# Performance work log

Measured on AMD Instinct MI355X. Metric: run time of the kernel, lower is better.

## Reference

```python
import jax, jax.numpy as jnp
import numpy as np

N, NFEAT, NHID, NCLASS, NHEADS = 4096, 512, 64, 40, 8
ALPHA = 0.2
NEG = -9e15


def setup_inputs() -> dict:
    key = jax.random.key(0)
    ks = jax.random.split(key, 6)
    x = jax.random.normal(ks[0], (N, NFEAT), dtype=jnp.float32)
    adj = jax.random.randint(ks[1], (2, N, N), 0, 2, dtype=jnp.int32)
    # Xavier-ish scaled params
    W1 = jax.random.normal(ks[2], (NHEADS, NFEAT, NHID), dtype=jnp.float32) * (1.0 / np.sqrt(NFEAT))
    a1 = jax.random.normal(ks[3], (NHEADS, 2, NHID), dtype=jnp.float32) * (1.0 / np.sqrt(2 * NHID))
    Wo = jax.random.normal(ks[4], (NHEADS * NHID, NCLASS), dtype=jnp.float32) * (1.0 / np.sqrt(NHEADS * NHID))
    ao = jax.random.normal(ks[5], (2, NCLASS), dtype=jnp.float32) * (1.0 / np.sqrt(2 * NCLASS))
    return {"x": x, "adj": adj, "W1": W1, "a1": a1, "Wo": Wo, "ao": ao}


def _gat_layer(h, adj_mask, W, a_src, a_dst, concat):
    # h: [N,F]; W: [...,F,F']; a_src/a_dst: [...,F']
    if W.ndim == 3:  # multi-head: [H,F,F']
        Wh = jnp.einsum('nf,hfd->hnd', h, W)              # [H,N,F']
        f1 = jnp.einsum('hnd,hd->hn', Wh, a_src)           # [H,N]
        f2 = jnp.einsum('hnd,hd->hn', Wh, a_dst)
        e = jax.nn.leaky_relu(f1[:, :, None] + f2[:, None, :], ALPHA)  # [H,N,N]
        e = jnp.where(adj_mask[None], e, NEG)
        att = jax.nn.softmax(e, axis=-1)
        out = jnp.einsum('hnm,hmd->hnd', att, Wh)          # [H,N,F']
    else:
        Wh = h @ W                                         # [N,F']
        f1 = Wh @ a_src
        f2 = Wh @ a_dst
        e = jax.nn.leaky_relu(f1[:, None] + f2[None, :], ALPHA)
        e = jnp.where(adj_mask, e, NEG)
        att = jax.nn.softmax(e, axis=-1)
        out = att @ Wh
    return jax.nn.elu(out) if concat else out


def reference(x, adj, W1, a1, Wo, ao):
    adj1 = adj[1] > 0
    adj0 = adj[0] > 0
    # layer 1: NHEADS heads, concat=True
    h = _gat_layer(x, adj1, W1, a1[:, 0], a1[:, 1], concat=True)   # [H,N,NHID]
    h = jnp.transpose(h, (1, 0, 2)).reshape(x.shape[0], -1)        # [N, H*NHID]
    # output layer: concat=False, then outer ELU + log_softmax
    out = _gat_layer(h, adj0, Wo, ao[0], ao[1], concat=False)      # [N, NCLASS]
    out = jax.nn.elu(out)
    return jax.nn.log_softmax(out, axis=1)
```

## Files before the change

kernel.cpp:

```cpp
#include <hip/hip_runtime.h>
#include <hip/hip_bf16.h>

#define N      4096
#define NFEAT  512
#define NHID   64
#define NHEADS 8
#define NCLASS 40
#define ALPHA  0.2f

typedef unsigned short u16;
typedef unsigned int   u32;
typedef __attribute__((ext_vector_type(8))) short bf16x8;
typedef __attribute__((ext_vector_type(4))) float f32x4;

__device__ __forceinline__ float lrelu(float v) {
    return v > 0.f ? v : ALPHA * v;
}
__device__ __forceinline__ u16 f2b(float f) {
    u32 u = __float_as_uint(f);
    return (u16)((u + 0x7FFFu + ((u >> 16) & 1u)) >> 16);
}

__global__ __launch_bounds__(256) void k1_gemm1(const float* __restrict__ x,
                                                const float* __restrict__ W1,
                                                float* __restrict__ Wh1) {
    __shared__ float As[16][64];
    __shared__ float Bs[16][64];
    const int t  = threadIdx.x;
    const int n0 = blockIdx.x * 64;
    const int h  = blockIdx.y;
    const int ti = t >> 4, tj = t & 15;
    const int an = t >> 2;
    const int af = (t & 3) * 4;
    const int bf = t >> 4;
    const int bd = (t & 15) * 4;
    float acc[4][4] = {};
    for (int f0 = 0; f0 < NFEAT; f0 += 16) {
        __syncthreads();
        float4 av = *(const float4*)&x[(size_t)(n0 + an) * NFEAT + f0 + af];
        As[af + 0][an] = av.x;
        As[af + 1][an] = av.y;
        As[af + 2][an] = av.z;
        As[af + 3][an] = av.w;
        *(float4*)&Bs[bf][bd] =
            *(const float4*)&W1[(size_t)h * NFEAT * NHID + (size_t)(f0 + bf) * NHID + bd];
        __syncthreads();
        #pragma unroll
        for (int kf = 0; kf < 16; ++kf) {
            float4 a4 = *(const float4*)&As[kf][ti * 4];
            float4 b4 = *(const float4*)&Bs[kf][tj * 4];
            acc[0][0] += a4.x * b4.x; acc[0][1] += a4.x * b4.y; acc[0][2] += a4.x * b4.z; acc[0][3] += a4.x * b4.w;
            acc[1][0] += a4.y * b4.x; acc[1][1] += a4.y * b4.y; acc[1][2] += a4.y * b4.z; acc[1][3] += a4.y * b4.w;
            acc[2][0] += a4.z * b4.x; acc[2][1] += a4.z * b4.y; acc[2][2] += a4.z * b4.z; acc[2][3] += a4.z * b4.w;
            acc[3][0] += a4.w * b4.x; acc[3][1] += a4.w * b4.y; acc[3][2] += a4.w * b4.z; acc[3][3] += a4.w * b4.w;
        }
    }
    #pragma unroll
    for (int i = 0; i < 4; ++i) {
        *(float4*)&Wh1[(size_t)(n0 + ti * 4 + i) * (NHEADS * NHID) + h * NHID + tj * 4] =
            make_float4(acc[i][0], acc[i][1], acc[i][2], acc[i][3]);
    }
}

__global__ __launch_bounds__(256) void k2_f12(const float* __restrict__ Wh1,
                                              const float* __restrict__ a1,
                                              float* __restrict__ f1,
                                              float* __restrict__ f2) {
    const int t = threadIdx.x;
    const int lane = t & 63;
    const int u = blockIdx.x * 4 + (t >> 6);
    const int h = u >> 12;
    const int n = u & (N - 1);
    float v  = Wh1[(size_t)n * 512 + h * 64 + lane];
    float s1 = v * a1[h * 128 + lane];
    float s2 = v * a1[h * 128 + 64 + lane];
    #pragma unroll
    for (int off = 32; off >= 1; off >>= 1) {
        s1 += __shfl_xor(s1, off);
        s2 += __shfl_xor(s2, off);
    }
    if (lane == 0) { f1[h * N + n] = s1; f2[h * N + n] = s2; }
}

__global__ __launch_bounds__(256) void k2t_transpose(const float* __restrict__ Wh1,
                                                     u16* __restrict__ Wh1T) {
    __shared__ float ts[64 * 68];
    const int t  = threadIdx.x;
    const int m0 = blockIdx.x * 64;
    const int h  = blockIdx.y;
    #pragma unroll
    for (int i = 0; i < 4; ++i) {
        int flat = t + 256 * i;
        int row = flat >> 4;
        int c4  = (flat & 15) * 4;
        *(float4*)&ts[row * 68 + c4] =
            *(const float4*)&Wh1[(size_t)(m0 + row) * 512 + h * 64 + c4];
    }
    __syncthreads();
    const int d  = t >> 2;
    const int ms = (t & 3) * 16;
    u32 p[8];
    #pragma unroll
    for (int j = 0; j < 8; ++j) {
        float v0 = ts[(ms + 2 * j) * 68 + d];
        float v1 = ts[(ms + 2 * j + 1) * 68 + d];
        p[j] = (u32)f2b(v0) | ((u32)f2b(v1) << 16);
    }
    u32* dst = (u32*)&Wh1T[((size_t)(h * 64 + d)) * 4096 + m0 + ms];
    *(uint4*)dst       = make_uint4(p[0], p[1], p[2], p[3]);
    *(uint4*)(dst + 4) = make_uint4(p[4], p[5], p[6], p[7]);
}

__global__ __launch_bounds__(256, 4) void k3_attn1(const int* __restrict__ adj1,
                                                   const u16* __restrict__ Wh1T,
                                                   const float* __restrict__ f1,
                                                   const float* __restrict__ f2,
                                                   float* __restrict__ pacc1,
                                                   float* __restrict__ pz1) {
    __shared__ u16  wbf[64 * 136];
    __shared__ u16  whT[80 * 136];
    __shared__ float f1s[64];
    const int t     = threadIdx.x;
    const int n0    = blockIdx.x * 64;
    const int h     = blockIdx.y;
    const int chunk = blockIdx.z;
    const int lane  = t & 63;
    const int wrow  = (t >> 6) * 16;
    const int c4    = (t & 31) * 4;
    const int rg    = t >> 5;
    if (t < 64) f1s[t] = f1[h * N + n0 + t];
    #pragma unroll
    for (int i = 0; i < 9; ++i) {
        int flat = t + 256 * i;
        if (flat < 16 * 136) {
            int row = 64 + flat / 136;
            whT[row * 136 + (flat % 136)] = (row == 64) ? (u16)0x3F80 : (u16)0;
        }
    }
    f32x4 acc[5];
    #pragma unroll
    for (int df = 0; df < 5; ++df)
        #pragma unroll
        for (int r = 0; r < 4; ++r) acc[df][r] = 0.f;
    __syncthreads();

    const int mbeg = chunk * 2048;
    for (int m0 = mbeg; m0 < mbeg + 2048; m0 += 128) {
        float4 f2v = *(const float4*)&f2[h * N + m0 + c4];
        #pragma unroll
        for (int i = 0; i < 8; ++i) {
            int rr = rg + 8 * i;
            int4 a4 = *(const int4*)&adj1[(size_t)(n0 + rr) * N + m0 + c4];
            float f1v = f1s[rr];
            float w0 = a4.x ? __expf(lrelu(f1v + f2v.x)) : 0.f;
            float w1 = a4.y ? __expf(lrelu(f1v + f2v.y)) : 0.f;
            float w2 = a4.z ? __expf(lrelu(f1v + f2v.z)) : 0.f;
            float w3 = a4.w ? __expf(lrelu(f1v + f2v.w)) : 0.f;
            uint2 pk;
            pk.x = (u32)f2b(w0) | ((u32)f2b(w1) << 16);
            pk.y = (u32)f2b(w2) | ((u32)f2b(w3) << 16);
            *(uint2*)&wbf[rr * 136 + c4] = pk;
        }
        #pragma unroll
        for (int i = 0; i < 4; ++i) {
            int flat = t + 256 * i;
            int row = flat >> 4;
            int c8  = (flat & 15) * 8;
            *(uint4*)&whT[row * 136 + c8] =
                *(const uint4*)&Wh1T[((size_t)(h * 64 + row)) * 4096 + m0 + c8];
        }
        __syncthreads();
        const int ar   = wrow + (lane & 15);
        const int koff = (lane >> 4) * 8;
        #pragma unroll
        for (int ks = 0; ks < 4; ++ks) {
            int k0 = ks * 32 + koff;
            bf16x8 a = *(const bf16x8*)&wbf[ar * 136 + k0];
            #pragma unroll
            for (int df = 0; df < 5; ++df) {
                bf16x8 b = *(const bf16x8*)&whT[(df * 16 + (lane & 15)) * 136 + k0];
                acc[df] = __builtin_amdgcn_mfma_f32_16x16x32_bf16(a, b, acc[df], 0, 0, 0);
            }
        }
        __syncthreads();
    }
    const size_t rowbase = (size_t)(chunk * 8 + h) * 4096 + n0;
    #pragma unroll
    for (int r = 0; r < 4; ++r) {
        int nl = wrow + (lane >> 4) * 4 + r;
        float z = __shfl(acc[4][r], lane & 48);
        if ((lane & 15) == 0) pz1[rowbase + nl] = z;
        #pragma unroll
        for (int df = 0; df < 4; ++df)
            pacc1[(rowbase + nl) * 64 + df * 16 + (lane & 15)] = acc[df][r];
    }
}

__global__ __launch_bounds__(256) void k3b_norm(const float* __restrict__ pacc1,
                                                const float* __restrict__ pz1,
                                                float* __restrict__ h1) {
    const int g = blockIdx.x * 256 + threadIdx.x;
    const int d = g & 63;
    const int h = (g >> 6) & 7;
    const int n = g >> 9;
    const size_t i0 = (size_t)h * 4096 + n;
    float s = pacc1[i0 * 64 + d] + pacc1[(i0 + 8 * 4096) * 64 + d];
    float z = pz1[i0] + pz1[i0 + 8 * 4096];
    float v = s / fmaxf(z, 1e-30f);
    h1[(size_t)n * 512 + h * 64 + d] = v > 0.f ? v : __expf(v) - 1.f;
}

__global__ __launch_bounds__(256) void k4_gemm2(const float* __restrict__ h1,
                                                const float* __restrict__ Wo,
                                                float* __restrict__ Wh2) {
    const int t = threadIdx.x;
    const int c = t & 63;
    const int n = blockIdx.x * 4 + (t >> 6);
    if (c < NCLASS) {
        const float* hrow = &h1[(size_t)n * 512];
        float acc = 0.f;
        #pragma unroll 8
        for (int f = 0; f < 512; ++f)
            acc += hrow[f] * Wo[f * NCLASS + c];
        Wh2[(size_t)n * NCLASS + c] = acc;
    }
}

__global__ __launch_bounds__(256) void k4b_fo(const float* __restrict__ Wh2,
                                              const float* __restrict__ ao,
                                              float* __restrict__ f1o,
                                              float* __restrict__ f2o,
                                              u16* __restrict__ Wh2T) {
    const int n = blockIdx.x * 256 + threadIdx.x;
    float s1 = 0.f, s2 = 0.f;
    #pragma unroll
    for (int c = 0; c < NCLASS; ++c) {
        float v = Wh2[(size_t)n * NCLASS + c];
        s1 += v * ao[c];
        s2 += v * ao[NCLASS + c];
        Wh2T[(size_t)c * 4096 + n] = f2b(v);
    }
    f1o[n] = s1; f2o[n] = s2;
}

__global__ __launch_bounds__(256, 4) void k5a_attn2(const int* __restrict__ adj0,
                                                    const u16* __restrict__ Wh2T,
                                                    const float* __restrict__ f1o,
                                                    const float* __restrict__ f2o,
                                                    float* __restrict__ pacc,
                                                    float* __restrict__ pz) {
    __shared__ u16  wbf[64 * 136];
    __shared__ u16  whT[64 * 136];
    __shared__ float f1s[64];
    const int t     = threadIdx.x;
    const int n0    = blockIdx.x * 64;
    const int chunk = blockIdx.y;
    const int mbase = chunk * 256;
    const int lane  = t & 63;
    const int wrow  = (t >> 6) * 16;
    const int c4    = (t & 31) * 4;
    const int rg    = t >> 5;
    if (t < 64) f1s[t] = f1o[n0 + t];
    #pragma unroll
    for (int i = 0; i < 13; ++i) {
        int flat = t + 256 * i;
        if (flat < 24 * 136) {
            int row = 40 + flat / 136;
            whT[row * 136 + (flat % 136)] = (row == 48) ? (u16)0x3F80 : (u16)0;
        }
    }
    f32x4 acc[4];
    #pragma unroll
    for (int df = 0; df < 4; ++df)
        #pragma unroll
        for (int r = 0; r < 4; ++r) acc[df][r] = 0.f;
    __syncthreads();

    for (int mt = 0; mt < 2; ++mt) {
        int m0 = mbase + mt * 128;
        float4 f2v = *(const float4*)&f2o[m0 + c4];
        #pragma unroll
        for (int i = 0; i < 8; ++i) {
            int rr = rg + 8 * i;
            int4 a4 = *(const int4*)&adj0[(size_t)(n0 + rr) * N + m0 + c4];
            float f1v = f1s[rr];
            float w0 = a4.x ? __expf(lrelu(f1v + f2v.x)) : 0.f;
            float w1 = a4.y ? __expf(lrelu(f1v + f2v.y)) : 0.f;
            float w2 = a4.z ? __expf(lrelu(f1v + f2v.z)) : 0.f;
            float w3 = a4.w ? __expf(lrelu(f1v + f2v.w)) : 0.f;
            uint2 pk;
            pk.x = (u32)f2b(w0) | ((u32)f2b(w1) << 16);
            pk.y = (u32)f2b(w2) | ((u32)f2b(w3) << 16);
            *(uint2*)&wbf[rr * 136 + c4] = pk;
        }
        #pragma unroll
        for (int i = 0; i < 3; ++i) {
            int flat = t + 256 * i;
            if (flat < 640) {
                int row = flat >> 4;
                int c8  = (flat & 15) * 8;
                *(uint4*)&whT[row * 136 + c8] =
                    *(const uint4*)&Wh2T[(size_t)row * 4096 + m0 + c8];
            }
        }
        __syncthreads();
        const int ar   = wrow + (lane & 15);
        const int koff = (lane >> 4) * 8;
        #pragma unroll
        for (int ks = 0; ks < 4; ++ks) {
            int k0 = ks * 32 + koff;
            bf16x8 a = *(const bf16x8*)&wbf[ar * 136 + k0];
            #pragma unroll
            for (int df = 0; df < 4; ++df) {
                bf16x8 b = *(const bf16x8*)&whT[(df * 16 + (lane & 15)) * 136 + k0];
                acc[df] = __builtin_amdgcn_mfma_f32_16x16x32_bf16(a, b, acc[df], 0, 0, 0);
            }
        }
        __syncthreads();
    }
    #pragma unroll
    for (int r = 0; r < 4; ++r) {
        int n = n0 + wrow + (lane >> 4) * 4 + r;
        float z = __shfl(acc[3][r], lane & 48);
        if ((lane & 15) == 0) pz[(size_t)chunk * N + n] = z;
        #pragma unroll
        for (int df = 0; df < 3; ++df) {
            int c = df * 16 + (lane & 15);
            if (c < NCLASS)
                pacc[((size_t)chunk * N + n) * NCLASS + c] = acc[df][r];
        }
    }
}

__global__ __launch_bounds__(256) void k5b_final(const float* __restrict__ pacc,
                                                 const float* __restrict__ pz,
                                                 float* __restrict__ out) {
    const int t = threadIdx.x;
    const int lane = t & 63;
    const int n = blockIdx.x * 4 + (t >> 6);
    float s = 0.f, Z = 0.f;
    #pragma unroll
    for (int ch = 0; ch < 16; ++ch) {
        Z += pz[(size_t)ch * N + n];
        if (lane < NCLASS) s += pacc[((size_t)ch * N + n) * NCLASS + lane];
    }
    float v;
    if (lane < NCLASS) {
        v = s / fmaxf(Z, 1e-30f);
        v = v > 0.f ? v : __expf(v) - 1.f;
    } else {
        v = -INFINITY;
    }
    float mx = v;
    #pragma unroll
    for (int off = 32; off >= 1; off >>= 1) mx = fmaxf(mx, __shfl_xor(mx, off));
    float ex = (lane < NCLASS) ? __expf(v - mx) : 0.f;
    #pragma unroll
    for (int off = 32; off >= 1; off >>= 1) ex += __shfl_xor(ex, off);
    float lse = mx + __logf(ex);
    if (lane < NCLASS) out[(size_t)n * NCLASS + lane] = v - lse;
}

extern "C" void kernel_launch(void* const* d_in, const int* in_sizes, int n_in,
                              void* d_out, int out_size, void* d_ws, size_t ws_size,
                              hipStream_t stream) {
    const float* x   = (const float*)d_in[0];
    const int*   adj = (const int*)d_in[1];
    const float* W1  = (const float*)d_in[2];
    const float* a1  = (const float*)d_in[3];
    const float* Wo  = (const float*)d_in[4];
    const float* ao  = (const float*)d_in[5];

    float* ws    = (float*)d_ws;
    float* h1    = ws;
    float* f1    = h1 + 2097152;
    float* f2    = f1 + 32768;
    float* Wh2   = f2 + 32768;
    float* f1o   = Wh2 + 163840;
    float* f2o   = f1o + 4096;
    float* pz    = f2o + 4096;
    float* pz1   = pz + 65536;
    u16*   Wh1T  = (u16*)(pz1 + 65536);
    u16*   Wh2T  = Wh1T + 2097152;
    float* R     = (float*)(Wh2T + 163840);
    float* Wh1   = R;
    float* pacc1 = R;
    float* pacc  = R;

    const int* adj0 = adj;
    const int* adj1 = adj + (size_t)N * N;

    hipLaunchKernelGGL(k1_gemm1,      dim3(64, 8),    dim3(256), 0, stream, x, W1, Wh1);
    hipLaunchKernelGGL(k2_f12,        dim3(8192),     dim3(256), 0, stream, Wh1, a1, f1, f2);
    hipLaunchKernelGGL(k2t_transpose, dim3(64, 8),    dim3(256), 0, stream, Wh1, Wh1T);
    hipLaunchKernelGGL(k3_attn1,      dim3(64, 8, 2), dim3(256), 0, stream, adj1, Wh1T, f1, f2, pacc1, pz1);
    hipLaunchKernelGGL(k3b_norm,      dim3(8192),     dim3(256), 0, stream, pacc1, pz1, h1);
    hipLaunchKernelGGL(k4_gemm2,      dim3(1024),     dim3(256), 0, stream, h1, Wo, Wh2);
    hipLaunchKernelGGL(k4b_fo,        dim3(16),       dim3(256), 0, stream, Wh2, ao, f1o, f2o, Wh2T);
    hipLaunchKernelGGL(k5a_attn2,     dim3(64, 16),   dim3(256), 0, stream, adj0, Wh2T, f1o, f2o, pacc, pz);
    hipLaunchKernelGGL(k5b_final,     dim3(1024),     dim3(256), 0, stream, pacc, pz, (float*)d_out);
}
```

Measured before the change: 348.4 us.

## Move first GEMM to bf16 MFMA and compute attention weights in registers

The first-layer projection now runs as a bf16 MFMA GEMM on pre-converted x and W1, writing the transposed bf16 Wh1T directly. This replaces the fp32 FMA GEMM and the separate transpose pass, and f1/f2 are then read from Wh1T. Both attention kernels build their exp weights straight into MFMA A-operand registers instead of staging them through shared memory. They also prefetch the Wh tile into registers before the barrier, use exp2 with LOG2E folded into the logits, and raise the occupancy hint to 5. The cost is that the projection is now computed in bf16 instead of fp32, adding rounding error, and two extra conversion kernels are launched.

```diff
diff --git a/kernel.cpp b/kernel.cpp
--- a/kernel.cpp
+++ b/kernel.cpp
@@ -7,86 +7,44 @@
 #define NHEADS 8
 #define NCLASS 40
 #define ALPHA  0.2f
+#define LOG2E  1.44269504f
 
 typedef unsigned short u16;
 typedef unsigned int   u32;
 typedef __attribute__((ext_vector_type(8))) short bf16x8;
 typedef __attribute__((ext_vector_type(4))) float f32x4;
 
-__device__ __forceinline__ float lrelu(float v) {
-    return v > 0.f ? v : ALPHA * v;
+__device__ __forceinline__ float b2f(u16 u) {
+    return __uint_as_float(((u32)u) << 16);
+}
+__device__ __forceinline__ u32 rnd_hi(float f) {
+    u32 u = __float_as_uint(f);
+    return u + 0x7FFFu + ((u >> 16) & 1u);
+}
+__device__ __forceinline__ u32 pkbf(float lo, float hi) {
+    return __builtin_amdgcn_perm(rnd_hi(hi), rnd_hi(lo), 0x07060302);
 }
 __device__ __forceinline__ u16 f2b(float f) {
-    u32 u = __float_as_uint(f);
-    return (u16)((u + 0x7FFFu + ((u >> 16) & 1u)) >> 16);
-}
-
-__global__ __launch_bounds__(256) void k1_gemm1(const float* __restrict__ x,
-                                                const float* __restrict__ W1,
-                                                float* __restrict__ Wh1) {
-    __shared__ float As[16][64];
-    __shared__ float Bs[16][64];
-    const int t  = threadIdx.x;
-    const int n0 = blockIdx.x * 64;
-    const int h  = blockIdx.y;
-    const int ti = t >> 4, tj = t & 15;
-    const int an = t >> 2;
-    const int af = (t & 3) * 4;
-    const int bf = t >> 4;
-    const int bd = (t & 15) * 4;
-    float acc[4][4] = {};
-    for (int f0 = 0; f0 < NFEAT; f0 += 16) {
-        __syncthreads();
-        float4 av = *(const float4*)&x[(size_t)(n0 + an) * NFEAT + f0 + af];
-        As[af + 0][an] = av.x;
-        As[af + 1][an] = av.y;
-        As[af + 2][an] = av.z;
-        As[af + 3][an] = av.w;
-        *(float4*)&Bs[bf][bd] =
-            *(const float4*)&W1[(size_t)h * NFEAT * NHID + (size_t)(f0 + bf) * NHID + bd];
-        __syncthreads();
-        #pragma unroll
-        for (int kf = 0; kf < 16; ++kf) {
-            float4 a4 = *(const float4*)&As[kf][ti * 4];
-            float4 b4 = *(const float4*)&Bs[kf][tj * 4];
-            acc[0][0] += a4.x * b4.x; acc[0][1] += a4.x * b4.y; acc[0][2] += a4.x * b4.z; acc[0][3] += a4.x * b4.w;
-            acc[1][0] += a4.y * b4.x; acc[1][1] += a4.y * b4.y; acc[1][2] += a4.y * b4.z; acc[1][3] += a4.y * b4.w;
-            acc[2][0] += a4.z * b4.x; acc[2][1] += a4.z * b4.y; acc[2][2] += a4.z * b4.z; acc[2][3] += a4.z * b4.w;
-            acc[3][0] += a4.w * b4.x; acc[3][1] += a4.w * b4.y; acc[3][2] += a4.w * b4.z; acc[3][3] += a4.w * b4.w;
-        }
-    }
-    #pragma unroll
-    for (int i = 0; i < 4; ++i) {
-        *(float4*)&Wh1[(size_t)(n0 + ti * 4 + i) * (NHEADS * NHID) + h * NHID + tj * 4] =
-            make_float4(acc[i][0], acc[i][1], acc[i][2], acc[i][3]);
-    }
-}
-
-__global__ __launch_bounds__(256) void k2_f12(const float* __restrict__ Wh1,
-                                              const float* __restrict__ a1,
-                                              float* __restrict__ f1,
-                                              float* __restrict__ f2) {
-    const int t = threadIdx.x;
-    const int lane = t & 63;
-    const int u = blockIdx.x * 4 + (t >> 6);
-    const int h = u >> 12;
-    const int n = u & (N - 1);
-    float v  = Wh1[(size_t)n * 512 + h * 64 + lane];
-    float s1 = v * a1[h * 128 + lane];
-    float s2 = v * a1[h * 128 + 64 + lane];
-    #pragma unroll
-    for (int off = 32; off >= 1; off >>= 1) {
-        s1 += __shfl_xor(s1, off);
-        s2 += __shfl_xor(s2, off);
-    }
-    if (lane == 0) { f1[h * N + n] = s1; f2[h * N + n] = s2; }
-}
-
-__global__ __launch_bounds__(256) void k2t_transpose(const float* __restrict__ Wh1,
-                                                     u16* __restrict__ Wh1T) {
+    return (u16)(rnd_hi(f) >> 16);
+}
+
+__global__ __launch_bounds__(256) void kcx(const float* __restrict__ x,
+                                           u16* __restrict__ xb) {
+    const int g = blockIdx.x * 256 + threadIdx.x;
+    const size_t base = (size_t)g * 8;
+    float4 v0 = *(const float4*)&x[base];
+    float4 v1 = *(const float4*)&x[base + 4];
+    uint4 o;
+    o.x = pkbf(v0.x, v0.y); o.y = pkbf(v0.z, v0.w);
+    o.z = pkbf(v1.x, v1.y); o.w = pkbf(v1.z, v1.w);
+    *(uint4*)&xb[base] = o;
+}
+
+__global__ __launch_bounds__(256) void kcw(const float* __restrict__ W1,
+                                           u16* __restrict__ W1b) {
     __shared__ float ts[64 * 68];
     const int t  = threadIdx.x;
-    const int m0 = blockIdx.x * 64;
+    const int f0 = blockIdx.x * 64;
     const int h  = blockIdx.y;
     #pragma unroll
     for (int i = 0; i < 4; ++i) {
@@ -94,41 +52,111 @@
         int row = flat >> 4;
         int c4  = (flat & 15) * 4;
         *(float4*)&ts[row * 68 + c4] =
-            *(const float4*)&Wh1[(size_t)(m0 + row) * 512 + h * 64 + c4];
+            *(const float4*)&W1[((size_t)h * 512 + f0 + row) * 64 + c4];
     }
     __syncthreads();
     const int d  = t >> 2;
-    const int ms = (t & 3) * 16;
+    const int fs = (t & 3) * 16;
     u32 p[8];
     #pragma unroll
-    for (int j = 0; j < 8; ++j) {
-        float v0 = ts[(ms + 2 * j) * 68 + d];
-        float v1 = ts[(ms + 2 * j + 1) * 68 + d];
-        p[j] = (u32)f2b(v0) | ((u32)f2b(v1) << 16);
-    }
-    u32* dst = (u32*)&Wh1T[((size_t)(h * 64 + d)) * 4096 + m0 + ms];
+    for (int j = 0; j < 8; ++j)
+        p[j] = pkbf(ts[(fs + 2 * j) * 68 + d], ts[(fs + 2 * j + 1) * 68 + d]);
+    u32* dst = (u32*)&W1b[((size_t)(h * 64 + d)) * 512 + f0 + fs];
     *(uint4*)dst       = make_uint4(p[0], p[1], p[2], p[3]);
     *(uint4*)(dst + 4) = make_uint4(p[4], p[5], p[6], p[7]);
 }
 
-__global__ __launch_bounds__(256, 4) void k3_attn1(const int* __restrict__ adj1,
+__global__ __launch_bounds__(256, 4) void k1m_gemm1(const u16* __restrict__ xb,
+                                                    const u16* __restrict__ W1b,
+                                                    u16* __restrict__ Wh1T) {
+    __shared__ u16 xs[64 * 72];
+    __shared__ u16 wvs[64 * 72];
+    const int t    = threadIdx.x;
+    const int n0   = blockIdx.x * 64;
+    const int h    = blockIdx.y;
+    const int lane = t & 63;
+    const int l15  = lane & 15;
+    const int q    = lane >> 4;
+    const int wrow = (t >> 6) * 16;
+    f32x4 acc[4];
+    #pragma unroll
+    for (int df = 0; df < 4; ++df)
+        #pragma unroll
+        for (int r = 0; r < 4; ++r) acc[df][r] = 0.f;
+    for (int f0 = 0; f0 < 512; f0 += 64) {
+        uint4 sx[2], sw[2];
+        #pragma unroll
+        for (int i = 0; i < 2; ++i) {
+            int flat = t + 256 * i;
+            int row = flat >> 3;
+            int c8  = (flat & 7) * 8;
+            sx[i] = *(const uint4*)&xb[(size_t)(n0 + row) * 512 + f0 + c8];
+            sw[i] = *(const uint4*)&W1b[((size_t)(h * 64 + row)) * 512 + f0 + c8];
+        }
+        __syncthreads();
+        #pragma unroll
+        for (int i = 0; i < 2; ++i) {
+            int flat = t + 256 * i;
+            int row = flat >> 3;
+            int c8  = (flat & 7) * 8;
+            *(uint4*)&xs[row * 72 + c8]  = sx[i];
+            *(uint4*)&wvs[row * 72 + c8] = sw[i];
+        }
+        __syncthreads();
+        #pragma unroll
+        for (int ks = 0; ks < 2; ++ks) {
+            int k0 = ks * 32 + q * 8;
+            bf16x8 a = *(const bf16x8*)&xs[(wrow + l15) * 72 + k0];
+            #pragma unroll
+            for (int df = 0; df < 4; ++df) {
+                bf16x8 b = *(const bf16x8*)&wvs[(df * 16 + l15) * 72 + k0];
+                acc[df] = __builtin_amdgcn_mfma_f32_16x16x32_bf16(a, b, acc[df], 0, 0, 0);
+            }
+        }
+    }
+    #pragma unroll
+    for (int df = 0; df < 4; ++df) {
+        uint2 o;
+        o.x = pkbf(acc[df][0], acc[df][1]);
+        o.y = pkbf(acc[df][2], acc[df][3]);
+        *(uint2*)&Wh1T[((size_t)(h * 64 + df * 16 + l15)) * 4096 + n0 + wrow + q * 4] = o;
+    }
+}
+
+__global__ __launch_bounds__(256) void k2_f12(const u16* __restrict__ Wh1T,
+                                              const float* __restrict__ a1,
+                                              float* __restrict__ F1,
+                                              float* __restrict__ F2) {
+    const int g = blockIdx.x * 256 + threadIdx.x;
+    const int h = g >> 12;
+    const int n = g & 4095;
+    float s1 = 0.f, s2 = 0.f;
+    #pragma unroll 8
+    for (int d = 0; d < 64; ++d) {
+        float v = b2f(Wh1T[((size_t)(h * 64 + d)) * 4096 + n]);
+        s1 += v * a1[h * 128 + d];
+        s2 += v * a1[h * 128 + 64 + d];
+    }
+    F1[h * 4096 + n] = s1 * LOG2E;
+    F2[h * 4096 + n] = s2 * LOG2E;
+}
+
+__global__ __launch_bounds__(256, 5) void k3_attn1(const int* __restrict__ adj1,
                                                    const u16* __restrict__ Wh1T,
-                                                   const float* __restrict__ f1,
-                                                   const float* __restrict__ f2,
+                                                   const float* __restrict__ F1,
+                                                   const float* __restrict__ F2,
                                                    float* __restrict__ pacc1,
                                                    float* __restrict__ pz1) {
-    __shared__ u16  wbf[64 * 136];
-    __shared__ u16  whT[80 * 136];
-    __shared__ float f1s[64];
+    __shared__ u16 whT[80 * 136];
     const int t     = threadIdx.x;
     const int n0    = blockIdx.x * 64;
     const int h     = blockIdx.y;
     const int chunk = blockIdx.z;
     const int lane  = t & 63;
+    const int l15   = lane & 15;
+    const int q     = lane >> 4;
     const int wrow  = (t >> 6) * 16;
-    const int c4    = (t & 31) * 4;
-    const int rg    = t >> 5;
-    if (t < 64) f1s[t] = f1[h * N + n0 + t];
+    const int ar    = wrow + l15;
     #pragma unroll
     for (int i = 0; i < 9; ++i) {
         int flat = t + 256 * i;
@@ -142,57 +170,71 @@
     for (int df = 0; df < 5; ++df)
         #pragma unroll
         for (int r = 0; r < 4; ++r) acc[df][r] = 0.f;
+    const float F1v = F1[h * N + n0 + ar];
     __syncthreads();
 
     const int mbeg = chunk * 2048;
     for (int m0 = mbeg; m0 < mbeg + 2048; m0 += 128) {
-        float4 f2v = *(const float4*)&f2[h * N + m0 + c4];
-        #pragma unroll
-        for (int i = 0; i < 8; ++i) {
-            int rr = rg + 8 * i;
-            int4 a4 = *(const int4*)&adj1[(size_t)(n0 + rr) * N + m0 + c4];
-            float f1v = f1s[rr];
-            float w0 = a4.x ? __expf(lrelu(f1v + f2v.x)) : 0.f;
-            float w1 = a4.y ? __expf(lrelu(f1v + f2v.y)) : 0.f;
-            float w2 = a4.z ? __expf(lrelu(f1v + f2v.z)) : 0.f;
-            float w3 = a4.w ? __expf(lrelu(f1v + f2v.w)) : 0.f;
-            uint2 pk;
-            pk.x = (u32)f2b(w0) | ((u32)f2b(w1) << 16);
-            pk.y = (u32)f2b(w2) | ((u32)f2b(w3) << 16);
-            *(uint2*)&wbf[rr * 136 + c4] = pk;
-        }
+        uint4 st[4];
         #pragma unroll
         for (int i = 0; i < 4; ++i) {
             int flat = t + 256 * i;
             int row = flat >> 4;
             int c8  = (flat & 15) * 8;
-            *(uint4*)&whT[row * 136 + c8] =
-                *(const uint4*)&Wh1T[((size_t)(h * 64 + row)) * 4096 + m0 + c8];
-        }
-        __syncthreads();
-        const int ar   = wrow + (lane & 15);
-        const int koff = (lane >> 4) * 8;
+            st[i] = *(const uint4*)&Wh1T[((size_t)(h * 64 + row)) * 4096 + m0 + c8];
+        }
+        const int*   ap = &adj1[(size_t)(n0 + ar) * N + m0 + q * 8];
+        const float* fp = &F2[h * N + m0 + q * 8];
+        bf16x8 aw[4];
         #pragma unroll
         for (int ks = 0; ks < 4; ++ks) {
-            int k0 = ks * 32 + koff;
-            bf16x8 a = *(const bf16x8*)&wbf[ar * 136 + k0];
+            int4   a0 = *(const int4*)(ap + ks * 32);
+            int4   a1v = *(const int4*)(ap + ks * 32 + 4);
+            float4 g0 = *(const float4*)(fp + ks * 32);
+            float4 g1 = *(const float4*)(fp + ks * 32 + 4);
+            float t0 = F1v + g0.x, t1 = F1v + g0.y, t2 = F1v + g0.z, t3 = F1v + g0.w;
+            float t4 = F1v + g1.x, t5 = F1v + g1.y, t6 = F1v + g1.z, t7 = F1v + g1.w;
+            float w0 = a0.x  ? exp2f(fmaxf(t0, ALPHA * t0)) : 0.f;
+            float w1 = a0.y  ? exp2f(fmaxf(t1, ALPHA * t1)) : 0.f;
+            float w2 = a0.z  ? exp2f(fmaxf(t2, ALPHA * t2)) : 0.f;
+            float w3 = a0.w  ? exp2f(fmaxf(t3, ALPHA * t3)) : 0.f;
+            float w4 = a1v.x ? exp2f(fmaxf(t4, ALPHA * t4)) : 0.f;
+            float w5 = a1v.y ? exp2f(fmaxf(t5, ALPHA * t5)) : 0.f;
+            float w6 = a1v.z ? exp2f(fmaxf(t6, ALPHA * t6)) : 0.f;
+            float w7 = a1v.w ? exp2f(fmaxf(t7, ALPHA * t7)) : 0.f;
+            union { u32 u[4]; bf16x8 v; } pk;
+            pk.u[0] = pkbf(w0, w1); pk.u[1] = pkbf(w2, w3);
+            pk.u[2] = pkbf(w4, w5); pk.u[3] = pkbf(w6, w7);
+            aw[ks] = pk.v;
+        }
+        __syncthreads();
+        #pragma unroll
+        for (int i = 0; i < 4; ++i) {
+            int flat = t + 256 * i;
+            int row = flat >> 4;
+            int c8  = (flat & 15) * 8;
+            *(uint4*)&whT[row * 136 + c8] = st[i];
+        }
+        __syncthreads();
+        #pragma unroll
+        for (int ks = 0; ks < 4; ++ks) {
+            int k0 = ks * 32 + q * 8;
             #pragma unroll
             for (int df = 0; df < 5; ++df) {
-                bf16x8 b = *(const bf16x8*)&whT[(df * 16 + (lane & 15)) * 136 + k0];
-                acc[df] = __builtin_amdgcn_mfma_f32_16x16x32_bf16(a, b, acc[df], 0, 0, 0);
+                bf16x8 b = *(const bf16x8*)&whT[(df * 16 + l15) * 136 + k0];
+                acc[df] = __builtin_amdgcn_mfma_f32_16x16x32_bf16(aw[ks], b, acc[df], 0, 0, 0);
             }
         }
-        __syncthreads();
     }
     const size_t rowbase = (size_t)(chunk * 8 + h) * 4096 + n0;
     #pragma unroll
     for (int r = 0; r < 4; ++r) {
-        int nl = wrow + (lane >> 4) * 4 + r;
+        int nl = wrow + q * 4 + r;
         float z = __shfl(acc[4][r], lane & 48);
-        if ((lane & 15) == 0) pz1[rowbase + nl] = z;
+        if (l15 == 0) pz1[rowbase + nl] = z;
         #pragma unroll
         for (int df = 0; df < 4; ++df)
-            pacc1[(rowbase + nl) * 64 + df * 16 + (lane & 15)] = acc[df][r];
+            pacc1[(rowbase + nl) * 64 + df * 16 + l15] = acc[df][r];
     }
 }
 
@@ -228,8 +270,8 @@
 
 __global__ __launch_bounds__(256) void k4b_fo(const float* __restrict__ Wh2,
                                               const float* __restrict__ ao,
-                                              float* __restrict__ f1o,
-                                              float* __restrict__ f2o,
+                                              float* __restrict__ F1o,
+                                              float* __restrict__ F2o,
                                               u16* __restrict__ Wh2T) {
     const int n = blockIdx.x * 256 + threadIdx.x;
     float s1 = 0.f, s2 = 0.f;
@@ -240,27 +282,26 @@
         s2 += v * ao[NCLASS + c];
         Wh2T[(size_t)c * 4096 + n] = f2b(v);
     }
-    f1o[n] = s1; f2o[n] = s2;
-}
-
-__global__ __launch_bounds__(256, 4) void k5a_attn2(const int* __restrict__ adj0,
+    F1o[n] = s1 * LOG2E;
+    F2o[n] = s2 * LOG2E;
+}
+
+__global__ __launch_bounds__(256, 5) void k5a_attn2(const int* __restrict__ adj0,
                                                     const u16* __restrict__ Wh2T,
-                                                    const float* __restrict__ f1o,
-                                                    const float* __restrict__ f2o,
+                                                    const float* __restrict__ F1o,
+                                                    const float* __restrict__ F2o,
                                                     float* __restrict__ pacc,
                                                     float* __restrict__ pz) {
-    __shared__ u16  wbf[64 * 136];
-    __shared__ u16  whT[64 * 136];
-    __shared__ float f1s[64];
+    __shared__ u16 whT[64 * 136];
     const int t     = threadIdx.x;
     const int n0    = blockIdx.x * 64;
     const int chunk = blockIdx.y;
     const int mbase = chunk * 256;
     const int lane  = t & 63;
+    const int l15   = lane & 15;
+    const int q     = lane >> 4;
     const int wrow  = (t >> 6) * 16;
-    const int c4    = (t & 31) * 4;
-    const int rg    = t >> 5;
-    if (t < 64) f1s[t] = f1o[n0 + t];
+    const int ar    = wrow + l15;
     #pragma unroll
     for (int i = 0; i < 13; ++i) {
         int flat = t + 256 * i;
@@ -274,58 +315,74 @@
     for (int df = 0; df < 4; ++df)
         #pragma unroll
         for (int r = 0; r < 4; ++r) acc[df][r] = 0.f;
+    const float F1v = F1o[n0 + ar];
     __syncthreads();
 
     for (int mt = 0; mt < 2; ++mt) {
         int m0 = mbase + mt * 128;
-        float4 f2v = *(const float4*)&f2o[m0 + c4];
-        #pragma unroll
-        for (int i = 0; i < 8; ++i) {
-            int rr = rg + 8 * i;
-            int4 a4 = *(const int4*)&adj0[(size_t)(n0 + rr) * N + m0 + c4];
-            float f1v = f1s[rr];
-            float w0 = a4.x ? __expf(lrelu(f1v + f2v.x)) : 0.f;
-            float w1 = a4.y ? __expf(lrelu(f1v + f2v.y)) : 0.f;
-            float w2 = a4.z ? __expf(lrelu(f1v + f2v.z)) : 0.f;
-            float w3 = a4.w ? __expf(lrelu(f1v + f2v.w)) : 0.f;
-            uint2 pk;
-            pk.x = (u32)f2b(w0) | ((u32)f2b(w1) << 16);
-            pk.y = (u32)f2b(w2) | ((u32)f2b(w3) << 16);
-            *(uint2*)&wbf[rr * 136 + c4] = pk;
-        }
+        uint4 st[3];
         #pragma unroll
         for (int i = 0; i < 3; ++i) {
             int flat = t + 256 * i;
             if (flat < 640) {
                 int row = flat >> 4;
                 int c8  = (flat & 15) * 8;
-                *(uint4*)&whT[row * 136 + c8] =
-                    *(const uint4*)&Wh2T[(size_t)row * 4096 + m0 + c8];
+                st[i] = *(const uint4*)&Wh2T[(size_t)row * 4096 + m0 + c8];
             }
         }
-        __syncthreads();
-        const int ar   = wrow + (lane & 15);
-        const int koff = (lane >> 4) * 8;
+        const int*   ap = &adj0[(size_t)(n0 + ar) * N + m0 + q * 8];
+        const float* fp = &F2o[m0 + q * 8];
+        bf16x8 aw[4];
         #pragma unroll
         for (int ks = 0; ks < 4; ++ks) {
-            int k0 = ks * 32 + koff;
-            bf16x8 a = *(const bf16x8*)&wbf[ar * 136 + k0];
+            int4   a0 = *(const int4*)(ap + ks * 32);
+            int4   a1v = *(const int4*)(ap + ks * 32 + 4);
+            float4 g0 = *(const float4*)(fp + ks * 32);
+            float4 g1 = *(const float4*)(fp + ks * 32 + 4);
+            float t0 = F1v + g0.x, t1 = F1v + g0.y, t2 = F1v + g0.z, t3 = F1v + g0.w;
+            float t4 = F1v + g1.x, t5 = F1v + g1.y, t6 = F1v + g1.z, t7 = F1v + g1.w;
+            float w0 = a0.x  ? exp2f(fmaxf(t0, ALPHA * t0)) : 0.f;
+            float w1 = a0.y  ? exp2f(fmaxf(t1, ALPHA * t1)) : 0.f;
+            float w2 = a0.z  ? exp2f(fmaxf(t2, ALPHA * t2)) : 0.f;
+            float w3 = a0.w  ? exp2f(fmaxf(t3, ALPHA * t3)) : 0.f;
+            float w4 = a1v.x ? exp2f(fmaxf(t4, ALPHA * t4)) : 0.f;
+            float w5 = a1v.y ? exp2f(fmaxf(t5, ALPHA * t5)) : 0.f;
+            float w6 = a1v.z ? exp2f(fmaxf(t6, ALPHA * t6)) : 0.f;
+            float w7 = a1v.w ? exp2f(fmaxf(t7, ALPHA * t7)) : 0.f;
+            union { u32 u[4]; bf16x8 v; } pk;
+            pk.u[0] = pkbf(w0, w1); pk.u[1] = pkbf(w2, w3);
+            pk.u[2] = pkbf(w4, w5); pk.u[3] = pkbf(w6, w7);
+            aw[ks] = pk.v;
+        }
+        __syncthreads();
+        #pragma unroll
+        for (int i = 0; i < 3; ++i) {
+            int flat = t + 256 * i;
+            if (flat < 640) {
+                int row = flat >> 4;
+                int c8  = (flat & 15) * 8;
+                *(uint4*)&whT[row * 136 + c8] = st[i];
+            }
+        }
+        __syncthreads();
+        #pragma unroll
+        for (int ks = 0; ks < 4; ++ks) {
+            int k0 = ks * 32 + q * 8;
             #pragma unroll
             for (int df = 0; df < 4; ++df) {
-                bf16x8 b = *(const bf16x8*)&whT[(df * 16 + (lane & 15)) * 136 + k0];
-                acc[df] = __builtin_amdgcn_mfma_f32_16x16x32_bf16(a, b, acc[df], 0, 0, 0);
+                bf16x8 b = *(const bf16x8*)&whT[(df * 16 + l15) * 136 + k0];
+                acc[df] = __builtin_amdgcn_mfma_f32_16x16x32_bf16(aw[ks], b, acc[df], 0, 0, 0);
             }
         }
-        __syncthreads();
     }
     #pragma unroll
     for (int r = 0; r < 4; ++r) {
-        int n = n0 + wrow + (lane >> 4) * 4 + r;
+        int n = n0 + wrow + q * 4 + r;
         float z = __shfl(acc[3][r], lane & 48);
-        if ((lane & 15) == 0) pz[(size_t)chunk * N + n] = z;
+        if (l15 == 0) pz[(size_t)chunk * N + n] = z;
         #pragma unroll
         for (int df = 0; df < 3; ++df) {
-            int c = df * 16 + (lane & 15);
+            int c = df * 16 + l15;
             if (c < NCLASS)
                 pacc[((size_t)chunk * N + n) * NCLASS + c] = acc[df][r];
         }
@@ -373,30 +430,32 @@
 
     float* ws    = (float*)d_ws;
     float* h1    = ws;
-    float* f1    = h1 + 2097152;
-    float* f2    = f1 + 32768;
-    float* Wh2   = f2 + 32768;
-    float* f1o   = Wh2 + 163840;
-    float* f2o   = f1o + 4096;
-    float* pz    = f2o + 4096;
+    float* F1    = h1 + 2097152;
+    float* F2    = F1 + 32768;
+    float* Wh2   = F2 + 32768;
+    float* F1o   = Wh2 + 163840;
+    float* F2o   = F1o + 4096;
+    float* pz    = F2o + 4096;
     float* pz1   = pz + 65536;
     u16*   Wh1T  = (u16*)(pz1 + 65536);
     u16*   Wh2T  = Wh1T + 2097152;
     float* R     = (float*)(Wh2T + 163840);
-    float* Wh1   = R;
+    u16*   xb    = (u16*)R;
+    u16*   W1b   = xb + 2097152;
     float* pacc1 = R;
     float* pacc  = R;
 
     const int* adj0 = adj;
     const int* adj1 = adj + (size_t)N * N;
 
-    hipLaunchKernelGGL(k1_gemm1,      dim3(64, 8),    dim3(256), 0, stream, x, W1, Wh1);
-    hipLaunchKernelGGL(k2_f12,        dim3(8192),     dim3(256), 0, stream, Wh1, a1, f1, f2);
-    hipLaunchKernelGGL(k2t_transpose, dim3(64, 8),    dim3(256), 0, stream, Wh1, Wh1T);
-    hipLaunchKernelGGL(k3_attn1,      dim3(64, 8, 2), dim3(256), 0, stream, adj1, Wh1T, f1, f2, pacc1, pz1);
-    hipLaunchKernelGGL(k3b_norm,      dim3(8192),     dim3(256), 0, stream, pacc1, pz1, h1);
-    hipLaunchKernelGGL(k4_gemm2,      dim3(1024),     dim3(256), 0, stream, h1, Wo, Wh2);
-    hipLaunchKernelGGL(k4b_fo,        dim3(16),       dim3(256), 0, stream, Wh2, ao, f1o, f2o, Wh2T);
-    hipLaunchKernelGGL(k5a_attn2,     dim3(64, 16),   dim3(256), 0, stream, adj0, Wh2T, f1o, f2o, pacc, pz);
-    hipLaunchKernelGGL(k5b_final,     dim3(1024),     dim3(256), 0, stream, pacc, pz, (float*)d_out);
-}
+    hipLaunchKernelGGL(kcx,       dim3(1024),     dim3(256), 0, stream, x, xb);
+    hipLaunchKernelGGL(kcw,       dim3(8, 8),     dim3(256), 0, stream, W1, W1b);
+    hipLaunchKernelGGL(k1m_gemm1, dim3(64, 8),    dim3(256), 0, stream, xb, W1b, Wh1T);
+    hipLaunchKernelGGL(k2_f12,    dim3(128),      dim3(256), 0, stream, Wh1T, a1, F1, F2);
+    hipLaunchKernelGGL(k3_attn1,  dim3(64, 8, 2), dim3(256), 0, stream, adj1, Wh1T, F1, F2, pacc1, pz1);
+    hipLaunchKernelGGL(k3b_norm,  dim3(8192),     dim3(256), 0, stream, pacc1, pz1, h1);
+    hipLaunchKernelGGL(k4_gemm2,  dim3(1024),     dim3(256), 0, stream, h1, Wo, Wh2);
+    hipLaunchKernelGGL(k4b_fo,    dim3(16),       dim3(256), 0, stream, Wh2, ao, F1o, F2o, Wh2T);
+    hipLaunchKernelGGL(k5a_attn2, dim3(64, 16),   dim3(256), 0, stream, adj0, Wh2T, F1o, F2o, pacc, pz);
+    hipLaunchKernelGGL(k5b_final, dim3(1024),     dim3(256), 0, stream, pacc, pz, (float*)d_out);
+}
```

After: 509.6 us. 1.46x slower.
